# Optimization experiments

Hardware: AMD Instinct MI355X
Metric: run time of the kernel (lower is better)

## Reference

```python
import jax, jax.numpy as jnp
import numpy as np

N = 50000      # total nodes across batched subgraphs
E = 800000     # total edges
R = 4          # num_relations
G = 16         # number of graphs (questions) in batch
NODE_DIM = 128
QDIM = 768
RQ = 64        # reduced_qn_dim
RN = 64        # reduced_node_dim
H = 128        # hidden_dim
OUT = 64       # output_dim


def setup_inputs() -> dict:
    key = jax.random.key(0)
    ks = jax.random.split(key, 16)
    def lin(k, i, o):
        return jax.random.normal(k, (i, o), jnp.float32) / np.float32(np.sqrt(i))
    def rel(k, i, o):
        return jax.random.normal(k, (R, i, o), jnp.float32) / np.float32(np.sqrt(i))
    return {
        "x": jax.random.normal(ks[0], (N, NODE_DIM), jnp.float32),
        "edge_index": jax.random.randint(ks[1], (2, E), 0, N, dtype=jnp.int32),
        "edge_attr": jax.random.randint(ks[2], (E,), 0, R, dtype=jnp.int32),
        "batch": jnp.sort(jax.random.randint(ks[3], (N,), 0, G, dtype=jnp.int32)),
        "question_embedding": jax.random.normal(ks[4], (G, QDIM), jnp.float32),
        "qn_W": lin(ks[5], QDIM, RQ), "qn_b": jnp.zeros((RQ,), jnp.float32),
        "W0": rel(ks[6], NODE_DIM, RN), "root0": lin(ks[7], NODE_DIM, RN), "b0": jnp.zeros((RN,), jnp.float32),
        "W1": rel(ks[8], RN + RQ, H), "root1": lin(ks[9], RN + RQ, H), "b1": jnp.zeros((H,), jnp.float32),
        "W2": rel(ks[10], H, H), "root2": lin(ks[11], H, H), "b2": jnp.zeros((H,), jnp.float32),
        "W3": rel(ks[12], H, OUT), "root3": lin(ks[13], H, OUT), "b3": jnp.zeros((OUT,), jnp.float32),
    }


def rgcn_conv(x, src, dst, etype, W, root, b):
    """PyG RGCNConv: out_i = x_i @ root + b + sum_r mean_{j in N_r(i)} x_j @ W_r."""
    out = x @ root + b
    for r in range(R):
        h = x @ W[r]                                  # [N, out] transform-then-gather
        mask = (etype == r)
        msgs = jnp.where(mask[:, None], h[src], 0.0)  # [E, out]
        s = jax.ops.segment_sum(msgs, dst, num_segments=N)
        cnt = jax.ops.segment_sum(mask.astype(x.dtype), dst, num_segments=N)
        out = out + s / jnp.maximum(cnt, 1.0)[:, None]
    return out


def reference(x, edge_index, edge_attr, batch, question_embedding,
              qn_W, qn_b, W0, root0, b0, W1, root1, b1, W2, root2, b2, W3, root3, b3):
    src, dst = edge_index[0], edge_index[1]
    q = jax.nn.relu(question_embedding @ qn_W + qn_b)          # [G, RQ]
    h = jax.nn.relu(rgcn_conv(x, src, dst, edge_attr, W0, root0, b0))
    combined = jnp.concatenate([h, q[batch]], axis=1)          # [N, RN+RQ]
    h = jax.nn.relu(rgcn_conv(combined, src, dst, edge_attr, W1, root1, b1))
    h = jax.nn.relu(rgcn_conv(h, src, dst, edge_attr, W2, root2, b2))
    return rgcn_conv(h, src, dst, edge_attr, W3, root3, b3)
```

## Files before the change

### kernel.cpp

```cpp
#include <hip/hip_runtime.h>
#include <hip/hip_bf16.h>

#define NN 50000
#define EE 800000
#define GG 16
#define QD 768
#define NBUCK 196
#define EPB 4000

typedef __bf16 bf16x8 __attribute__((ext_vector_type(8)));
typedef float f32x4 __attribute__((ext_vector_type(4)));

static __device__ __forceinline__ float bflo(unsigned u) {
    union { unsigned v; float f; } c; c.v = u << 16; return c.f;
}
static __device__ __forceinline__ float bfhi(unsigned u) {
    union { unsigned v; float f; } c; c.v = u & 0xffff0000u; return c.f;
}


#define PB_CVT 6250
#define PB_W0  (PB_CVT + 160)
#define PB_W1  (PB_W0 + 320)
#define PB_W2  (PB_W1 + 320)
#define PB_W3  (PB_W2 + 160)
#define PB_Q   (PB_W3 + 16)

__global__ __launch_bounds__(256) void prep_all(
        const float* __restrict__ x, __hip_bfloat16* __restrict__ xb,
        const float* __restrict__ qe, const float* __restrict__ qn_W,
        const float* __restrict__ qn_b, float* __restrict__ q,
        const float* __restrict__ W0, const float* __restrict__ root0, __hip_bfloat16* __restrict__ W5T0,
        const float* __restrict__ W1, const float* __restrict__ root1, __hip_bfloat16* __restrict__ W5T1,
        const float* __restrict__ W2, const float* __restrict__ root2, __hip_bfloat16* __restrict__ W5T2,
        const float* __restrict__ W3, const float* __restrict__ root3, __hip_bfloat16* __restrict__ W5T3) {
    __shared__ float red[256];
    int blk = blockIdx.x, tid = threadIdx.x;
    if (blk < PB_CVT) {
        int i = blk * 256 + tid;
        float4 v = ((const float4*)x)[i];
        union { ushort4 u; __hip_bfloat16 h[4]; } o;
        o.h[0] = __float2bfloat16(v.x); o.h[1] = __float2bfloat16(v.y);
        o.h[2] = __float2bfloat16(v.z); o.h[3] = __float2bfloat16(v.w);
        ((ushort4*)xb)[i] = o.u;
    } else if (blk < PB_W3) {
        const float* W; const float* root; __hip_bfloat16* WT; int O, base;
        if (blk < PB_W0)      { W = W0; root = root0; WT = W5T0; O = 64;  base = PB_CVT; }
        else if (blk < PB_W1) { W = W1; root = root1; WT = W5T1; O = 128; base = PB_W0; }
        else if (blk < PB_W2) { W = W2; root = root2; WT = W5T2; O = 128; base = PB_W1; }
        else                  { W = W3; root = root3; WT = W5T3; O = 64;  base = PB_W2; }
        int idx = (blk - base) * 256 + tid;
        int o = idx / 640, k = idx - o * 640;
        float v;
        if (k < 128) v = root[(size_t)k * O + o];
        else { int r = (k - 128) >> 7, kk = (k - 128) & 127; v = W[((size_t)r * 128 + kk) * O + o]; }
        WT[idx] = __float2bfloat16(v);
    } else {
        int g = blk - PB_W3;
        int o = tid & 63, kc = tid >> 6;
        const float* qr = qe + (size_t)g * QD;
        float s = 0.f;
        int k0 = kc * 192;
        for (int k = k0; k < k0 + 192; ++k)
            s = fmaf(qr[k], qn_W[(size_t)k * 64 + o], s);
        red[tid] = s;
        __syncthreads();
        if (tid < 64) {
            float t = red[tid] + red[tid + 64] + red[tid + 128] + red[tid + 192] + qn_b[o];
            q[g * 64 + o] = fmaxf(t, 0.f);
        }
    }
}


__global__ void bucket_hist(const int* __restrict__ dst, int* __restrict__ bcnt) {
    __shared__ int h[NBUCK];
    int tid = threadIdx.x;
    for (int i = tid; i < NBUCK; i += 256) h[i] = 0;
    __syncthreads();
    for (int e = blockIdx.x * 256 + tid; e < EE; e += gridDim.x * 256)
        atomicAdd(&h[dst[e] >> 8], 1);
    __syncthreads();
    for (int i = tid; i < NBUCK; i += 256) if (h[i]) atomicAdd(&bcnt[i], h[i]);
}

__global__ void bucket_scan(const int* __restrict__ bcnt, int* __restrict__ bbase,
                            int* __restrict__ bcur) {
    __shared__ int wt[4];
    int tid = threadIdx.x, lane = tid & 63, w = tid >> 6;
    int v = (tid < NBUCK) ? bcnt[tid] : 0;
    int sc = v;
#pragma unroll
    for (int off = 1; off < 64; off <<= 1) {
        int t = __shfl_up(sc, off, 64);
        if (lane >= off) sc += t;
    }
    if (lane == 63) wt[w] = sc;
    __syncthreads();
    int wbase = 0;
    for (int ww = 0; ww < w; ++ww) wbase += wt[ww];
    int excl = wbase + sc - v;
    if (tid <= NBUCK) bbase[tid] = excl;
    if (tid < NBUCK) bcur[tid] = excl;
}

__global__ __launch_bounds__(256) void bin_edges(const int* __restrict__ src,
                                                 const int* __restrict__ dst,
                                                 const int* __restrict__ et,
                                                 int* __restrict__ bcur,
                                                 unsigned* __restrict__ binned) {
    __shared__ int lcnt[NBUCK];
    __shared__ int lbase[NBUCK];
    int tid = threadIdx.x;
    int e0 = blockIdx.x * EPB, e1 = min(e0 + EPB, EE);
    for (int base = e0; base < e1; base += 2048) {
        for (int i = tid; i < NBUCK; i += 256) lcnt[i] = 0;
        __syncthreads();
        unsigned ent[8]; int bk[8], rk[8];
#pragma unroll
        for (int k = 0; k < 8; ++k) {
            int e = base + k * 256 + tid;
            if (e < e1) {
                int d = dst[e];
                bk[k] = d >> 8;
                ent[k] = ((unsigned)src[e] << 10) | ((unsigned)et[e] << 8) | (unsigned)(d & 255);
                rk[k] = atomicAdd(&lcnt[bk[k]], 1);
            } else bk[k] = -1;
        }
        __syncthreads();
        for (int i = tid; i < NBUCK; i += 256)
            lbase[i] = lcnt[i] ? atomicAdd(&bcur[i], lcnt[i]) : 0;
        __syncthreads();
#pragma unroll
        for (int k = 0; k < 8; ++k)
            if (bk[k] >= 0) binned[lbase[bk[k]] + rk[k]] = ent[k];
        __syncthreads();
    }
}

__global__ __launch_bounds__(256) void csr_fine(const int* __restrict__ bbase,
                                                const unsigned* __restrict__ binned,
                                                int* __restrict__ csr,
                                                int* __restrict__ offsets,
                                                int4* __restrict__ cnt4) {
    __shared__ int cnt[1024];
    __shared__ int wt[4];
    int b = blockIdx.x, tid = threadIdx.x, lane = tid & 63, w = tid >> 6;
    int seg0 = bbase[b], seg1 = bbase[b + 1];
    for (int i = tid; i < 1024; i += 256) cnt[i] = 0;
    __syncthreads();
    for (int e = seg0 + tid; e < seg1; e += 256) {
        unsigned u = binned[e];
        atomicAdd(&cnt[(u & 255) * 4 + ((u >> 8) & 3)], 1);
    }
    __syncthreads();
    int c0 = cnt[tid * 4], c1 = cnt[tid * 4 + 1], c2 = cnt[tid * 4 + 2], c3 = cnt[tid * 4 + 3];
    int s = c0 + c1 + c2 + c3;
    int sc = s;
#pragma unroll
    for (int off = 1; off < 64; off <<= 1) {
        int t = __shfl_up(sc, off, 64);
        if (lane >= off) sc += t;
    }
    if (lane == 63) wt[w] = sc;
    __syncthreads();
    int wbase = 0;
    for (int ww = 0; ww < w; ++ww) wbase += wt[ww];
    int excl = wbase + sc - s;
    cnt[tid * 4]     = excl;
    cnt[tid * 4 + 1] = excl + c0;
    cnt[tid * 4 + 2] = excl + c0 + c1;
    cnt[tid * 4 + 3] = excl + c0 + c1 + c2;
    int node = b * 256 + tid;
    if (node < NN) {
        offsets[node] = seg0 + excl;
        cnt4[node] = make_int4(c0, c1, c2, c3);
    }
    if (b == NBUCK - 1 && tid == 0) offsets[NN] = EE;
    __syncthreads();
    for (int e = seg0 + tid; e < seg1; e += 256) {
        unsigned u = binned[e];
        int r = atomicAdd(&cnt[(u & 255) * 4 + ((u >> 8) & 3)], 1);
        csr[seg0 + r] = (int)(((u >> 10) << 2) | ((u >> 8) & 3));
    }
}


__global__ __launch_bounds__(256) void agg_x(const __hip_bfloat16* __restrict__ X,
                                             const int* __restrict__ offsets,
                                             const int4* __restrict__ cnt4,
                                             const int* __restrict__ csr,
                                             const float* __restrict__ zpage,
                                             __hip_bfloat16* __restrict__ X5agg) {
    int lane = threadIdx.x & 63;
    int node = __builtin_amdgcn_readfirstlane(blockIdx.x * 4 + (threadIdx.x >> 6));
    const char* xb = (const char*)X;
    const char* zp = (const char*)zpage;
    int e0 = offsets[node];
    int4 c4 = cnt4[node];
    int st[4];
    st[0] = 0; st[1] = c4.x; st[2] = st[1] + c4.y; st[3] = st[2] + c4.z;
    int cs[4] = {c4.x, c4.y, c4.z, c4.w};
    int maxc = max(max(cs[0], cs[1]), max(cs[2], cs[3]));
    float aL[4] = {0.f, 0.f, 0.f, 0.f}, aH[4] = {0.f, 0.f, 0.f, 0.f};
    for (int i = 0; i < maxc; i += 2) {
        const char* bp[8];
#pragma unroll
        for (int jj = 0; jj < 2; ++jj) {
            int i2 = i + jj;
#pragma unroll
            for (int r = 0; r < 4; ++r) {
                int p = csr[min(e0 + st[r] + i2, EE - 1)];
                bp[jj * 4 + r] = (i2 < cs[r]) ? xb + (size_t)(p >> 2) * 256 : zp;
            }
        }
        unsigned u[8];
#pragma unroll
        for (int k = 0; k < 8; ++k)
            u[k] = *(const unsigned*)(bp[k] + lane * 4);
#pragma unroll
        for (int k = 0; k < 8; ++k) {
            int r = k & 3;
            aL[r] += bflo(u[k]);
            aH[r] += bfhi(u[k]);
        }
    }
    char* x5 = (char*)X5agg;
#pragma unroll
    for (int r = 0; r < 4; ++r) {
        float iv = 1.f / fmaxf((float)cs[r], 1.f);
        __hip_bfloat16 g0 = __float2bfloat16(aL[r] * iv);
        __hip_bfloat16 g1 = __float2bfloat16(aH[r] * iv);
        ushort2 pkd;
        pkd.x = *(unsigned short*)&g0; pkd.y = *(unsigned short*)&g1;
        *(ushort2*)(x5 + (size_t)node * 1024 + r * 256 + lane * 4) = pkd;
    }
}


template <int O, int MODE>
__global__ __launch_bounds__(256) void dense5(const __hip_bfloat16* __restrict__ Xself,
                                              const __hip_bfloat16* __restrict__ X5agg,
                                              const __hip_bfloat16* __restrict__ W5T,
                                              const float* __restrict__ bias,
                                              const float* __restrict__ q,
                                              const int* __restrict__ batch,
                                              __hip_bfloat16* __restrict__ xnext,
                                              float* __restrict__ out) {
    __shared__ char lds[16384];
    constexpr int NCT = O / 16;
    int tid = threadIdx.x;
    int wave = tid >> 6, lane = tid & 63;
    int quad = lane >> 4, l15 = lane & 15;
    int mbase = blockIdx.x * 128 + wave * 32;
    const __bf16* Ws = (const __bf16*)W5T;

    f32x4 acc[2][NCT];
#pragma unroll
    for (int mt = 0; mt < 2; ++mt)
#pragma unroll
        for (int t = 0; t < NCT; ++t) acc[mt][t] = f32x4{0, 0, 0, 0};

    int arow0 = min(mbase + l15, NN - 1);
    int arow1 = min(mbase + 16 + l15, NN - 1);
    const __bf16* aps0 = (const __bf16*)Xself + (size_t)arow0 * 128;
    const __bf16* aps1 = (const __bf16*)Xself + (size_t)arow1 * 128;
    const __bf16* apg0 = (const __bf16*)X5agg + (size_t)arow0 * 512;
    const __bf16* apg1 = (const __bf16*)X5agg + (size_t)arow1 * 512;

    for (int kc = 0; kc < 10; ++kc) {
        int k0 = kc * 64;
        const __bf16* a0base = (kc < 2) ? aps0 + kc * 64 : apg0 + (kc - 2) * 64;
        const __bf16* a1base = (kc < 2) ? aps1 + kc * 64 : apg1 + (kc - 2) * 64;
        __syncthreads();
        constexpr int NF = NCT * 2 * 64;
#pragma unroll
        for (int i = 0; i < NF / 256; ++i) {
            int f = tid + i * 256;
            int fl = f & 63;
            int o = (f >> 7) * 16 + (fl & 15);
            int kk = k0 + ((f >> 6) & 1) * 32 + ((fl >> 4) & 3) * 8;
            *(uint4*)(lds + f * 16) = *(const uint4*)(Ws + (size_t)o * 640 + kk);
        }
        __syncthreads();
#pragma unroll
        for (int ks = 0; ks < 2; ++ks) {
            bf16x8 a0 = *(const bf16x8*)(a0base + ks * 32 + quad * 8);
            bf16x8 a1 = *(const bf16x8*)(a1base + ks * 32 + quad * 8);
#pragma unroll
            for (int t = 0; t < NCT; ++t) {
                bf16x8 b = *(const bf16x8*)(lds + ((t * 2 + ks) * 64 + lane) * 16);
                acc[0][t] = __builtin_amdgcn_mfma_f32_16x16x32_bf16(a0, b, acc[0][t], 0, 0, 0);
                acc[1][t] = __builtin_amdgcn_mfma_f32_16x16x32_bf16(a1, b, acc[1][t], 0, 0, 0);
            }
        }
    }
    __syncthreads();

    if (MODE == 2) {
#pragma unroll
        for (int mt = 0; mt < 2; ++mt)
#pragma unroll
            for (int t = 0; t < NCT; ++t) {
                int col = t * 16 + l15;
                float bv = bias[col];
#pragma unroll
                for (int reg = 0; reg < 4; ++reg) {
                    int row = mbase + mt * 16 + quad * 4 + reg;
                    if (row < NN) out[(size_t)row * 64 + col] = acc[mt][t][reg] + bv;
                }
            }
        return;
    }

    __hip_bfloat16* tp = (__hip_bfloat16*)(lds + wave * 4096);
#pragma unroll
    for (int mt = 0; mt < 2; ++mt) {
        int m0 = mbase + mt * 16;
#pragma unroll
        for (int t = 0; t < NCT; ++t) {
            int col = t * 16 + l15;
            float bv = bias[col];
#pragma unroll
            for (int reg = 0; reg < 4; ++reg)
                tp[(quad * 4 + reg) * 128 + col] =
                    __float2bfloat16(fmaxf(acc[mt][t][reg] + bv, 0.f));
        }
        if (MODE == 0) {
            int row = lane >> 2;
            int cs = (lane & 3) * 16;
            int rnode = min(m0 + row, NN - 1);
            int g = batch[rnode];
#pragma unroll
            for (int i = 0; i < 4; ++i) {
                float4 v = *(const float4*)(q + g * 64 + cs + i * 4);
                __hip_bfloat16 q0 = __float2bfloat16(v.x), q1 = __float2bfloat16(v.y);
                __hip_bfloat16 q2 = __float2bfloat16(v.z), q3 = __float2bfloat16(v.w);
                ushort4 pk;
                pk.x = *(unsigned short*)&q0; pk.y = *(unsigned short*)&q1;
                pk.z = *(unsigned short*)&q2; pk.w = *(unsigned short*)&q3;
                *(ushort4*)(tp + row * 128 + 64 + cs + i * 4) = pk;
            }
        }
#pragma unroll
        for (int p = 0; p < 4; ++p) {
            int c = p * 64 + lane;
            int row = m0 + (c >> 4);
            if (row < NN)
                *(uint4*)((char*)xnext + (size_t)row * 256 + (c & 15) * 16) =
                    *(const uint4*)((const char*)tp + c * 16);
        }
    }
}


static inline size_t rup(size_t x) { return (x + 255) & ~(size_t)255; }

extern "C" void kernel_launch(void* const* d_in, const int* in_sizes, int n_in,
                              void* d_out, int out_size, void* d_ws, size_t ws_size,
                              hipStream_t stream) {
    const float* x      = (const float*)d_in[0];
    const int*   esrc   = (const int*)d_in[1];
    const int*   edst   = esrc + EE;
    const int*   eattr  = (const int*)d_in[2];
    const int*   batch  = (const int*)d_in[3];
    const float* qe     = (const float*)d_in[4];
    const float* qn_W   = (const float*)d_in[5];
    const float* qn_b   = (const float*)d_in[6];
    const float* W0 = (const float*)d_in[7],  *root0 = (const float*)d_in[8],  *b0 = (const float*)d_in[9];
    const float* W1 = (const float*)d_in[10], *root1 = (const float*)d_in[11], *b1 = (const float*)d_in[12];
    const float* W2 = (const float*)d_in[13], *root2 = (const float*)d_in[14], *b2 = (const float*)d_in[15];
    const float* W3 = (const float*)d_in[16], *root3 = (const float*)d_in[17], *b3 = (const float*)d_in[18];
    float* out = (float*)d_out;

    char* w = (char*)d_ws;
    float* q       = (float*)w;  w += rup(GG * 64 * 4);
    float* zpage   = (float*)w;  w += rup(256);
    int*   offsets = (int*)w;    w += rup(((size_t)NN + 1) * 4);
    int4*  cnt4    = (int4*)w;   w += rup((size_t)NN * 16);
    int*   bcnt    = (int*)w;    w += rup((size_t)NBUCK * 4);
    int*   bbase   = (int*)w;    w += rup(((size_t)NBUCK + 1) * 4);
    int*   bcur    = (int*)w;    w += rup((size_t)NBUCK * 4);
    unsigned* binned = (unsigned*)w; w += rup((size_t)EE * 4);
    int*   csr     = (int*)w;    w += rup((size_t)EE * 4);
    __hip_bfloat16* W5T0 = (__hip_bfloat16*)w; w += rup((size_t)64 * 640 * 2);
    __hip_bfloat16* W5T1 = (__hip_bfloat16*)w; w += rup((size_t)128 * 640 * 2);
    __hip_bfloat16* W5T2 = (__hip_bfloat16*)w; w += rup((size_t)128 * 640 * 2);
    __hip_bfloat16* W5T3 = (__hip_bfloat16*)w; w += rup((size_t)64 * 640 * 2);
    __hip_bfloat16* xb0 = (__hip_bfloat16*)w;  w += rup((size_t)NN * 128 * 2);
    __hip_bfloat16* xb1 = (__hip_bfloat16*)w;  w += rup((size_t)NN * 128 * 2);
    __hip_bfloat16* X5  = (__hip_bfloat16*)w;  w += rup((size_t)NN * 512 * 2);

    hipMemsetAsync(bcnt, 0, (size_t)NBUCK * 4, stream);
    hipMemsetAsync(zpage, 0, 256, stream);

    prep_all<<<PB_Q, 256, 0, stream>>>(x, xb0, qe, qn_W, qn_b, q,
                                       W0, root0, W5T0, W1, root1, W5T1,
                                       W2, root2, W5T2, W3, root3, W5T3);

    bucket_hist<<<256, 256, 0, stream>>>(edst, bcnt);
    bucket_scan<<<1, 256, 0, stream>>>(bcnt, bbase, bcur);
    bin_edges<<<(EE + EPB - 1) / EPB, 256, 0, stream>>>(esrc, edst, eattr, bcur, binned);
    csr_fine<<<NBUCK, 256, 0, stream>>>(bbase, binned, csr, offsets, cnt4);

    int aggblk = NN / 4;
    int dblk = (NN + 127) / 128;

    agg_x<<<aggblk, 256, 0, stream>>>(xb0, offsets, cnt4, csr, zpage, X5);
    dense5<64, 0><<<dblk, 256, 0, stream>>>(xb0, X5, W5T0, b0, q, batch, xb1, nullptr);

    agg_x<<<aggblk, 256, 0, stream>>>(xb1, offsets, cnt4, csr, zpage, X5);
    dense5<128, 1><<<dblk, 256, 0, stream>>>(xb1, X5, W5T1, b1, nullptr, nullptr, xb0, nullptr);

    agg_x<<<aggblk, 256, 0, stream>>>(xb0, offsets, cnt4, csr, zpage, X5);
    dense5<128, 1><<<dblk, 256, 0, stream>>>(xb0, X5, W5T2, b2, nullptr, nullptr, xb1, nullptr);

    agg_x<<<aggblk, 256, 0, stream>>>(xb1, offsets, cnt4, csr, zpage, X5);
    dense5<64, 2><<<dblk, 256, 0, stream>>>(xb1, X5, W5T3, b3, nullptr, nullptr, nullptr, out);
}
```

Measured before the change: 396.4 us.

## Fuse all phases into a persistent cooperative megakernel with grid syncs

Replaces the chain of separate kernel launches and memsets with one cooperative persistent kernel that loops over work with grid-stride loops and separates phases with grid.sync(). The aggregation loop now loads 64 CSR entries per wave at once and broadcasts them with readlane instead of reloading per edge. The dense stage appears retiled to 64-row tiles. Launch gaps and tail effects between phases should shrink, at the cost of grid-wide barriers, occupancy capped by the cooperative grid size, and register pressure from merging all phases into one kernel. A multi-kernel fallback is kept for when the cooperative launch fails.

Result: slower. 1.279 ms (+222.6%).

```diff
diff --git a/kernel.cpp b/kernel.cpp
--- a/kernel.cpp
+++ b/kernel.cpp
@@ -1,23 +1,16 @@
 #include <hip/hip_runtime.h>
 #include <hip/hip_bf16.h>
+#include <hip/hip_cooperative_groups.h>
+
+namespace cg = cooperative_groups;
 
 #define NN 50000
 #define EE 800000
 #define GG 16
 #define QD 768
 #define NBUCK 196
-#define EPB 4000
-
-typedef __bf16 bf16x8 __attribute__((ext_vector_type(8)));
-typedef float f32x4 __attribute__((ext_vector_type(4)));
-
-static __device__ __forceinline__ float bflo(unsigned u) {
-    union { unsigned v; float f; } c; c.v = u << 16; return c.f;
-}
-static __device__ __forceinline__ float bfhi(unsigned u) {
-    union { unsigned v; float f; } c; c.v = u & 0xffff0000u; return c.f;
-}
-
+#define NCHUNK ((EE + 2047) / 2048)
+#define NT64 ((NN + 63) / 64)
 
 #define PB_CVT 6250
 #define PB_W0  (PB_CVT + 160)
@@ -25,70 +18,89 @@
 #define PB_W2  (PB_W1 + 320)
 #define PB_W3  (PB_W2 + 160)
 #define PB_Q   (PB_W3 + 16)
-
-__global__ __launch_bounds__(256) void prep_all(
-        const float* __restrict__ x, __hip_bfloat16* __restrict__ xb,
-        const float* __restrict__ qe, const float* __restrict__ qn_W,
-        const float* __restrict__ qn_b, float* __restrict__ q,
-        const float* __restrict__ W0, const float* __restrict__ root0, __hip_bfloat16* __restrict__ W5T0,
-        const float* __restrict__ W1, const float* __restrict__ root1, __hip_bfloat16* __restrict__ W5T1,
-        const float* __restrict__ W2, const float* __restrict__ root2, __hip_bfloat16* __restrict__ W5T2,
-        const float* __restrict__ W3, const float* __restrict__ root3, __hip_bfloat16* __restrict__ W5T3) {
-    __shared__ float red[256];
-    int blk = blockIdx.x, tid = threadIdx.x;
-    if (blk < PB_CVT) {
-        int i = blk * 256 + tid;
-        float4 v = ((const float4*)x)[i];
-        union { ushort4 u; __hip_bfloat16 h[4]; } o;
-        o.h[0] = __float2bfloat16(v.x); o.h[1] = __float2bfloat16(v.y);
-        o.h[2] = __float2bfloat16(v.z); o.h[3] = __float2bfloat16(v.w);
-        ((ushort4*)xb)[i] = o.u;
-    } else if (blk < PB_W3) {
-        const float* W; const float* root; __hip_bfloat16* WT; int O, base;
-        if (blk < PB_W0)      { W = W0; root = root0; WT = W5T0; O = 64;  base = PB_CVT; }
-        else if (blk < PB_W1) { W = W1; root = root1; WT = W5T1; O = 128; base = PB_W0; }
-        else if (blk < PB_W2) { W = W2; root = root2; WT = W5T2; O = 128; base = PB_W1; }
-        else                  { W = W3; root = root3; WT = W5T3; O = 64;  base = PB_W2; }
-        int idx = (blk - base) * 256 + tid;
-        int o = idx / 640, k = idx - o * 640;
-        float v;
-        if (k < 128) v = root[(size_t)k * O + o];
-        else { int r = (k - 128) >> 7, kk = (k - 128) & 127; v = W[((size_t)r * 128 + kk) * O + o]; }
-        WT[idx] = __float2bfloat16(v);
-    } else {
-        int g = blk - PB_W3;
-        int o = tid & 63, kc = tid >> 6;
-        const float* qr = qe + (size_t)g * QD;
-        float s = 0.f;
-        int k0 = kc * 192;
-        for (int k = k0; k < k0 + 192; ++k)
-            s = fmaf(qr[k], qn_W[(size_t)k * 64 + o], s);
-        red[tid] = s;
-        __syncthreads();
-        if (tid < 64) {
-            float t = red[tid] + red[tid + 64] + red[tid + 128] + red[tid + 192] + qn_b[o];
-            q[g * 64 + o] = fmaxf(t, 0.f);
-        }
-    }
-}
-
-
-__global__ void bucket_hist(const int* __restrict__ dst, int* __restrict__ bcnt) {
-    __shared__ int h[NBUCK];
+#define PB_TOT (PB_Q + 1)
+
+typedef __bf16 bf16x8 __attribute__((ext_vector_type(8)));
+typedef float f32x4 __attribute__((ext_vector_type(4)));
+
+struct P {
+    const float* x; const int* esrc; const int* edst; const int* eattr; const int* batch;
+    const float* qe; const float* qn_W; const float* qn_b;
+    const float *W0, *root0, *b0, *W1, *root1, *b1, *W2, *root2, *b2, *W3, *root3, *b3;
+    float* out;
+    float* q; float* zpage; int* offsets; int4* cnt4; int* bcnt; int* bbase; int* bcur;
+    unsigned* binned; int* csr;
+    __hip_bfloat16 *W5T0, *W5T1, *W5T2, *W5T3, *xb0, *xb1, *X5;
+};
+
+static __device__ __forceinline__ float bflo(unsigned u) {
+    union { unsigned v; float f; } c; c.v = u << 16; return c.f;
+}
+static __device__ __forceinline__ float bfhi(unsigned u) {
+    union { unsigned v; float f; } c; c.v = u & 0xffff0000u; return c.f;
+}
+
+static __device__ void prep_phase(const P& p, char* smem) {
+    int tid = threadIdx.x;
+    for (int blk = blockIdx.x; blk < PB_TOT; blk += gridDim.x) {
+        if (blk < PB_CVT) {
+            int i = blk * 256 + tid;
+            float4 v = ((const float4*)p.x)[i];
+            union { ushort4 u; __hip_bfloat16 h[4]; } o;
+            o.h[0] = __float2bfloat16(v.x); o.h[1] = __float2bfloat16(v.y);
+            o.h[2] = __float2bfloat16(v.z); o.h[3] = __float2bfloat16(v.w);
+            ((ushort4*)p.xb0)[i] = o.u;
+        } else if (blk < PB_W3) {
+            const float* W; const float* root; __hip_bfloat16* WT; int O, base;
+            if (blk < PB_W0)      { W = p.W0; root = p.root0; WT = p.W5T0; O = 64;  base = PB_CVT; }
+            else if (blk < PB_W1) { W = p.W1; root = p.root1; WT = p.W5T1; O = 128; base = PB_W0; }
+            else if (blk < PB_W2) { W = p.W2; root = p.root2; WT = p.W5T2; O = 128; base = PB_W1; }
+            else                  { W = p.W3; root = p.root3; WT = p.W5T3; O = 64;  base = PB_W2; }
+            int idx = (blk - base) * 256 + tid;
+            int o = idx / 640, k = idx - o * 640;
+            float v;
+            if (k < 128) v = root[(size_t)k * O + o];
+            else { int r = (k - 128) >> 7, kk = (k - 128) & 127; v = W[((size_t)r * 128 + kk) * O + o]; }
+            WT[idx] = __float2bfloat16(v);
+        } else if (blk < PB_Q) {
+            float* red = (float*)smem;
+            int g = blk - PB_W3;
+            int o = tid & 63, kc = tid >> 6;
+            const float* qr = p.qe + (size_t)g * QD;
+            float s = 0.f;
+            int k0 = kc * 192;
+            for (int k = k0; k < k0 + 192; ++k)
+                s = fmaf(qr[k], p.qn_W[(size_t)k * 64 + o], s);
+            red[tid] = s;
+            __syncthreads();
+            if (tid < 64) {
+                float t = red[tid] + red[tid + 64] + red[tid + 128] + red[tid + 192] + p.qn_b[o];
+                p.q[g * 64 + o] = fmaxf(t, 0.f);
+            }
+            __syncthreads();
+        } else {
+            if (tid < NBUCK) p.bcnt[tid] = 0;
+            if (tid < 64) p.zpage[tid] = 0.f;
+        }
+    }
+}
+
+static __device__ void hist_phase(const P& p, char* smem) {
+    int* h = (int*)smem;
     int tid = threadIdx.x;
     for (int i = tid; i < NBUCK; i += 256) h[i] = 0;
     __syncthreads();
     for (int e = blockIdx.x * 256 + tid; e < EE; e += gridDim.x * 256)
-        atomicAdd(&h[dst[e] >> 8], 1);
+        atomicAdd(&h[p.edst[e] >> 8], 1);
     __syncthreads();
-    for (int i = tid; i < NBUCK; i += 256) if (h[i]) atomicAdd(&bcnt[i], h[i]);
-}
-
-__global__ void bucket_scan(const int* __restrict__ bcnt, int* __restrict__ bbase,
-                            int* __restrict__ bcur) {
-    __shared__ int wt[4];
+    for (int i = tid; i < NBUCK; i += 256) if (h[i]) atomicAdd(&p.bcnt[i], h[i]);
+    __syncthreads();
+}
+
+static __device__ void scan_phase(const P& p, char* smem) {
+    int* wt = (int*)smem;
     int tid = threadIdx.x, lane = tid & 63, w = tid >> 6;
-    int v = (tid < NBUCK) ? bcnt[tid] : 0;
+    int v = (tid < NBUCK) ? p.bcnt[tid] : 0;
     int sc = v;
 #pragma unroll
     for (int off = 1; off < 64; off <<= 1) {
@@ -100,20 +112,16 @@
     int wbase = 0;
     for (int ww = 0; ww < w; ++ww) wbase += wt[ww];
     int excl = wbase + sc - v;
-    if (tid <= NBUCK) bbase[tid] = excl;
-    if (tid < NBUCK) bcur[tid] = excl;
-}
-
-__global__ __launch_bounds__(256) void bin_edges(const int* __restrict__ src,
-                                                 const int* __restrict__ dst,
-                                                 const int* __restrict__ et,
-                                                 int* __restrict__ bcur,
-                                                 unsigned* __restrict__ binned) {
-    __shared__ int lcnt[NBUCK];
-    __shared__ int lbase[NBUCK];
+    if (tid <= NBUCK) p.bbase[tid] = excl;
+    if (tid < NBUCK) p.bcur[tid] = excl;
+}
+
+static __device__ void bin_phase(const P& p, char* smem) {
+    int* lcnt = (int*)smem;
+    int* lbase = lcnt + NBUCK;
     int tid = threadIdx.x;
-    int e0 = blockIdx.x * EPB, e1 = min(e0 + EPB, EE);
-    for (int base = e0; base < e1; base += 2048) {
+    for (int c = blockIdx.x; c < NCHUNK; c += gridDim.x) {
+        int base = c * 2048, e1 = min(base + 2048, EE);
         for (int i = tid; i < NBUCK; i += 256) lcnt[i] = 0;
         __syncthreads();
         unsigned ent[8]; int bk[8], rk[8];
@@ -121,236 +129,291 @@
         for (int k = 0; k < 8; ++k) {
             int e = base + k * 256 + tid;
             if (e < e1) {
-                int d = dst[e];
+                int d = p.edst[e];
                 bk[k] = d >> 8;
-                ent[k] = ((unsigned)src[e] << 10) | ((unsigned)et[e] << 8) | (unsigned)(d & 255);
+                ent[k] = ((unsigned)p.esrc[e] << 10) | ((unsigned)p.eattr[e] << 8) | (unsigned)(d & 255);
                 rk[k] = atomicAdd(&lcnt[bk[k]], 1);
             } else bk[k] = -1;
         }
         __syncthreads();
         for (int i = tid; i < NBUCK; i += 256)
-            lbase[i] = lcnt[i] ? atomicAdd(&bcur[i], lcnt[i]) : 0;
+            lbase[i] = lcnt[i] ? atomicAdd(&p.bcur[i], lcnt[i]) : 0;
         __syncthreads();
 #pragma unroll
         for (int k = 0; k < 8; ++k)
-            if (bk[k] >= 0) binned[lbase[bk[k]] + rk[k]] = ent[k];
-        __syncthreads();
-    }
-}
-
-__global__ __launch_bounds__(256) void csr_fine(const int* __restrict__ bbase,
-                                                const unsigned* __restrict__ binned,
-                                                int* __restrict__ csr,
-                                                int* __restrict__ offsets,
-                                                int4* __restrict__ cnt4) {
-    __shared__ int cnt[1024];
-    __shared__ int wt[4];
-    int b = blockIdx.x, tid = threadIdx.x, lane = tid & 63, w = tid >> 6;
-    int seg0 = bbase[b], seg1 = bbase[b + 1];
-    for (int i = tid; i < 1024; i += 256) cnt[i] = 0;
-    __syncthreads();
-    for (int e = seg0 + tid; e < seg1; e += 256) {
-        unsigned u = binned[e];
-        atomicAdd(&cnt[(u & 255) * 4 + ((u >> 8) & 3)], 1);
-    }
-    __syncthreads();
-    int c0 = cnt[tid * 4], c1 = cnt[tid * 4 + 1], c2 = cnt[tid * 4 + 2], c3 = cnt[tid * 4 + 3];
-    int s = c0 + c1 + c2 + c3;
-    int sc = s;
-#pragma unroll
-    for (int off = 1; off < 64; off <<= 1) {
-        int t = __shfl_up(sc, off, 64);
-        if (lane >= off) sc += t;
-    }
-    if (lane == 63) wt[w] = sc;
-    __syncthreads();
-    int wbase = 0;
-    for (int ww = 0; ww < w; ++ww) wbase += wt[ww];
-    int excl = wbase + sc - s;
-    cnt[tid * 4]     = excl;
-    cnt[tid * 4 + 1] = excl + c0;
-    cnt[tid * 4 + 2] = excl + c0 + c1;
-    cnt[tid * 4 + 3] = excl + c0 + c1 + c2;
-    int node = b * 256 + tid;
-    if (node < NN) {
-        offsets[node] = seg0 + excl;
-        cnt4[node] = make_int4(c0, c1, c2, c3);
-    }
-    if (b == NBUCK - 1 && tid == 0) offsets[NN] = EE;
-    __syncthreads();
-    for (int e = seg0 + tid; e < seg1; e += 256) {
-        unsigned u = binned[e];
-        int r = atomicAdd(&cnt[(u & 255) * 4 + ((u >> 8) & 3)], 1);
-        csr[seg0 + r] = (int)(((u >> 10) << 2) | ((u >> 8) & 3));
-    }
-}
-
-
-__global__ __launch_bounds__(256) void agg_x(const __hip_bfloat16* __restrict__ X,
-                                             const int* __restrict__ offsets,
-                                             const int4* __restrict__ cnt4,
-                                             const int* __restrict__ csr,
-                                             const float* __restrict__ zpage,
-                                             __hip_bfloat16* __restrict__ X5agg) {
+            if (bk[k] >= 0) p.binned[lbase[bk[k]] + rk[k]] = ent[k];
+        __syncthreads();
+    }
+}
+
+static __device__ void fine_phase(const P& p, char* smem) {
+    int* cnt = (int*)smem;
+    int* wt = cnt + 1024;
+    int tid = threadIdx.x, lane = tid & 63, w = tid >> 6;
+    for (int b = blockIdx.x; b < NBUCK; b += gridDim.x) {
+        int seg0 = p.bbase[b], seg1 = p.bbase[b + 1];
+        for (int i = tid; i < 1024; i += 256) cnt[i] = 0;
+        __syncthreads();
+        for (int e = seg0 + tid; e < seg1; e += 256) {
+            unsigned u = p.binned[e];
+            atomicAdd(&cnt[(u & 255) * 4 + ((u >> 8) & 3)], 1);
+        }
+        __syncthreads();
+        int c0 = cnt[tid * 4], c1 = cnt[tid * 4 + 1], c2 = cnt[tid * 4 + 2], c3 = cnt[tid * 4 + 3];
+        int s = c0 + c1 + c2 + c3;
+        int sc = s;
+#pragma unroll
+        for (int off = 1; off < 64; off <<= 1) {
+            int t = __shfl_up(sc, off, 64);
+            if (lane >= off) sc += t;
+        }
+        if (lane == 63) wt[w] = sc;
+        __syncthreads();
+        int wbase = 0;
+        for (int ww = 0; ww < w; ++ww) wbase += wt[ww];
+        int excl = wbase + sc - s;
+        cnt[tid * 4]     = excl;
+        cnt[tid * 4 + 1] = excl + c0;
+        cnt[tid * 4 + 2] = excl + c0 + c1;
+        cnt[tid * 4 + 3] = excl + c0 + c1 + c2;
+        int node = b * 256 + tid;
+        if (node < NN) {
+            p.offsets[node] = seg0 + excl;
+            p.cnt4[node] = make_int4(c0, c1, c2, c3);
+        }
+        if (b == NBUCK - 1 && tid == 0) p.offsets[NN] = EE;
+        __syncthreads();
+        for (int e = seg0 + tid; e < seg1; e += 256) {
+            unsigned u = p.binned[e];
+            int r = atomicAdd(&cnt[(u & 255) * 4 + ((u >> 8) & 3)], 1);
+            p.csr[seg0 + r] = (int)(((u >> 10) << 2) | ((u >> 8) & 3));
+        }
+        __syncthreads();
+    }
+}
+
+static __device__ void agg_phase(const __hip_bfloat16* X, const int* offsets,
+                                 const int4* cnt4, const int* csr,
+                                 const float* zpage, __hip_bfloat16* X5agg) {
     int lane = threadIdx.x & 63;
-    int node = __builtin_amdgcn_readfirstlane(blockIdx.x * 4 + (threadIdx.x >> 6));
+    int gw = blockIdx.x * 4 + (threadIdx.x >> 6);
     const char* xb = (const char*)X;
     const char* zp = (const char*)zpage;
-    int e0 = offsets[node];
-    int4 c4 = cnt4[node];
-    int st[4];
-    st[0] = 0; st[1] = c4.x; st[2] = st[1] + c4.y; st[3] = st[2] + c4.z;
-    int cs[4] = {c4.x, c4.y, c4.z, c4.w};
-    int maxc = max(max(cs[0], cs[1]), max(cs[2], cs[3]));
-    float aL[4] = {0.f, 0.f, 0.f, 0.f}, aH[4] = {0.f, 0.f, 0.f, 0.f};
-    for (int i = 0; i < maxc; i += 2) {
-        const char* bp[8];
-#pragma unroll
-        for (int jj = 0; jj < 2; ++jj) {
-            int i2 = i + jj;
-#pragma unroll
-            for (int r = 0; r < 4; ++r) {
-                int p = csr[min(e0 + st[r] + i2, EE - 1)];
-                bp[jj * 4 + r] = (i2 < cs[r]) ? xb + (size_t)(p >> 2) * 256 : zp;
-            }
-        }
-        unsigned u[8];
-#pragma unroll
-        for (int k = 0; k < 8; ++k)
-            u[k] = *(const unsigned*)(bp[k] + lane * 4);
-#pragma unroll
-        for (int k = 0; k < 8; ++k) {
-            int r = k & 3;
-            aL[r] += bflo(u[k]);
-            aH[r] += bfhi(u[k]);
-        }
-    }
-    char* x5 = (char*)X5agg;
-#pragma unroll
-    for (int r = 0; r < 4; ++r) {
-        float iv = 1.f / fmaxf((float)cs[r], 1.f);
-        __hip_bfloat16 g0 = __float2bfloat16(aL[r] * iv);
-        __hip_bfloat16 g1 = __float2bfloat16(aH[r] * iv);
-        ushort2 pkd;
-        pkd.x = *(unsigned short*)&g0; pkd.y = *(unsigned short*)&g1;
-        *(ushort2*)(x5 + (size_t)node * 1024 + r * 256 + lane * 4) = pkd;
-    }
-}
-
+    for (int n0 = gw; n0 < NN; n0 += gridDim.x * 4) {
+        int node = __builtin_amdgcn_readfirstlane(n0);
+        int e0 = __builtin_amdgcn_readfirstlane(offsets[node]);
+        int4 c4 = cnt4[node];
+        int cs[4];
+        cs[0] = __builtin_amdgcn_readfirstlane(c4.x);
+        cs[1] = __builtin_amdgcn_readfirstlane(c4.y);
+        cs[2] = __builtin_amdgcn_readfirstlane(c4.z);
+        cs[3] = __builtin_amdgcn_readfirstlane(c4.w);
+        int st[4];
+        st[0] = 0; st[1] = cs[0]; st[2] = st[1] + cs[1]; st[3] = st[2] + cs[2];
+        int maxc = max(max(cs[0], cs[1]), max(cs[2], cs[3]));
+        float aL[4] = {0.f, 0.f, 0.f, 0.f}, aH[4] = {0.f, 0.f, 0.f, 0.f};
+        for (int base = 0; base < maxc; base += 64) {
+            int pk[4];
+#pragma unroll
+            for (int r = 0; r < 4; ++r)
+                pk[r] = csr[min(e0 + st[r] + base + lane, EE - 1)];
+            int m = min(64, maxc - base);
+            for (int j = 0; j < m; j += 4) {
+                const char* bp[16];
+#pragma unroll
+                for (int jj = 0; jj < 4; ++jj) {
+                    int i = base + j + jj;
+#pragma unroll
+                    for (int r = 0; r < 4; ++r) {
+                        int pv = __builtin_amdgcn_readlane(pk[r], j + jj);
+                        bp[jj * 4 + r] = (i < cs[r]) ? xb + (size_t)(pv >> 2) * 256 : zp;
+                    }
+                }
+                unsigned u[16];
+#pragma unroll
+                for (int k = 0; k < 16; ++k)
+                    u[k] = *(const unsigned*)(bp[k] + lane * 4);
+#pragma unroll
+                for (int k = 0; k < 16; ++k) {
+                    int r = k & 3;
+                    aL[r] += bflo(u[k]);
+                    aH[r] += bfhi(u[k]);
+                }
+            }
+        }
+        char* x5 = (char*)X5agg;
+#pragma unroll
+        for (int r = 0; r < 4; ++r) {
+            float iv = 1.f / fmaxf((float)cs[r], 1.f);
+            __hip_bfloat16 g0 = __float2bfloat16(aL[r] * iv);
+            __hip_bfloat16 g1 = __float2bfloat16(aH[r] * iv);
+            ushort2 pkd;
+            pkd.x = *(unsigned short*)&g0; pkd.y = *(unsigned short*)&g1;
+            *(ushort2*)(x5 + (size_t)node * 1024 + r * 256 + lane * 4) = pkd;
+        }
+    }
+}
 
 template <int O, int MODE>
-__global__ __launch_bounds__(256) void dense5(const __hip_bfloat16* __restrict__ Xself,
-                                              const __hip_bfloat16* __restrict__ X5agg,
-                                              const __hip_bfloat16* __restrict__ W5T,
-                                              const float* __restrict__ bias,
-                                              const float* __restrict__ q,
-                                              const int* __restrict__ batch,
-                                              __hip_bfloat16* __restrict__ xnext,
-                                              float* __restrict__ out) {
-    __shared__ char lds[16384];
+static __device__ void dense_phase(const __hip_bfloat16* Xself, const __hip_bfloat16* X5agg,
+                                   const __hip_bfloat16* W5T, const float* bias,
+                                   const float* q, const int* batch,
+                                   __hip_bfloat16* xnext, float* out, char* lds) {
     constexpr int NCT = O / 16;
     int tid = threadIdx.x;
     int wave = tid >> 6, lane = tid & 63;
     int quad = lane >> 4, l15 = lane & 15;
-    int mbase = blockIdx.x * 128 + wave * 32;
     const __bf16* Ws = (const __bf16*)W5T;
-
-    f32x4 acc[2][NCT];
-#pragma unroll
-    for (int mt = 0; mt < 2; ++mt)
-#pragma unroll
-        for (int t = 0; t < NCT; ++t) acc[mt][t] = f32x4{0, 0, 0, 0};
-
-    int arow0 = min(mbase + l15, NN - 1);
-    int arow1 = min(mbase + 16 + l15, NN - 1);
-    const __bf16* aps0 = (const __bf16*)Xself + (size_t)arow0 * 128;
-    const __bf16* aps1 = (const __bf16*)Xself + (size_t)arow1 * 128;
-    const __bf16* apg0 = (const __bf16*)X5agg + (size_t)arow0 * 512;
-    const __bf16* apg1 = (const __bf16*)X5agg + (size_t)arow1 * 512;
-
-    for (int kc = 0; kc < 10; ++kc) {
-        int k0 = kc * 64;
-        const __bf16* a0base = (kc < 2) ? aps0 + kc * 64 : apg0 + (kc - 2) * 64;
-        const __bf16* a1base = (kc < 2) ? aps1 + kc * 64 : apg1 + (kc - 2) * 64;
-        __syncthreads();
-        constexpr int NF = NCT * 2 * 64;
-#pragma unroll
-        for (int i = 0; i < NF / 256; ++i) {
-            int f = tid + i * 256;
-            int fl = f & 63;
-            int o = (f >> 7) * 16 + (fl & 15);
-            int kk = k0 + ((f >> 6) & 1) * 32 + ((fl >> 4) & 3) * 8;
-            *(uint4*)(lds + f * 16) = *(const uint4*)(Ws + (size_t)o * 640 + kk);
-        }
-        __syncthreads();
-#pragma unroll
-        for (int ks = 0; ks < 2; ++ks) {
-            bf16x8 a0 = *(const bf16x8*)(a0base + ks * 32 + quad * 8);
-            bf16x8 a1 = *(const bf16x8*)(a1base + ks * 32 + quad * 8);
-#pragma unroll
-            for (int t = 0; t < NCT; ++t) {
-                bf16x8 b = *(const bf16x8*)(lds + ((t * 2 + ks) * 64 + lane) * 16);
-                acc[0][t] = __builtin_amdgcn_mfma_f32_16x16x32_bf16(a0, b, acc[0][t], 0, 0, 0);
-                acc[1][t] = __builtin_amdgcn_mfma_f32_16x16x32_bf16(a1, b, acc[1][t], 0, 0, 0);
-            }
-        }
-    }
-    __syncthreads();
-
-    if (MODE == 2) {
-#pragma unroll
-        for (int mt = 0; mt < 2; ++mt)
+    for (int tile = blockIdx.x; tile < NT64; tile += gridDim.x) {
+        int mbase = tile * 64 + wave * 16;
+        f32x4 acc[NCT];
+#pragma unroll
+        for (int t = 0; t < NCT; ++t) acc[t] = f32x4{0, 0, 0, 0};
+        int arow0 = min(mbase + l15, NN - 1);
+        const __bf16* aps0 = (const __bf16*)Xself + (size_t)arow0 * 128;
+        const __bf16* apg0 = (const __bf16*)X5agg + (size_t)arow0 * 512;
+        for (int kc = 0; kc < 10; ++kc) {
+            int k0 = kc * 64;
+            const __bf16* a0base = (kc < 2) ? aps0 + kc * 64 : apg0 + (kc - 2) * 64;
+            __syncthreads();
+            constexpr int NF = NCT * 2 * 64;
+#pragma unroll
+            for (int i = 0; i < NF / 256; ++i) {
+                int f = tid + i * 256;
+                int fl = f & 63;
+                int o = (f >> 7) * 16 + (fl & 15);
+                int kk = k0 + ((f >> 6) & 1) * 32 + ((fl >> 4) & 3) * 8;
+                *(uint4*)(lds + f * 16) = *(const uint4*)(Ws + (size_t)o * 640 + kk);
+            }
+            __syncthreads();
+#pragma unroll
+            for (int ks = 0; ks < 2; ++ks) {
+                bf16x8 a0 = *(const bf16x8*)(a0base + ks * 32 + quad * 8);
+#pragma unroll
+                for (int t = 0; t < NCT; ++t) {
+                    bf16x8 b = *(const bf16x8*)(lds + ((t * 2 + ks) * 64 + lane) * 16);
+                    acc[t] = __builtin_amdgcn_mfma_f32_16x16x32_bf16(a0, b, acc[t], 0, 0, 0);
+                }
+            }
+        }
+        __syncthreads();
+
+        if (MODE == 2) {
 #pragma unroll
             for (int t = 0; t < NCT; ++t) {
                 int col = t * 16 + l15;
                 float bv = bias[col];
 #pragma unroll
                 for (int reg = 0; reg < 4; ++reg) {
-                    int row = mbase + mt * 16 + quad * 4 + reg;
-                    if (row < NN) out[(size_t)row * 64 + col] = acc[mt][t][reg] + bv;
+                    int row = mbase + quad * 4 + reg;
+                    if (row < NN) out[(size_t)row * 64 + col] = acc[t][reg] + bv;
                 }
             }
-        return;
-    }
-
-    __hip_bfloat16* tp = (__hip_bfloat16*)(lds + wave * 4096);
-#pragma unroll
-    for (int mt = 0; mt < 2; ++mt) {
-        int m0 = mbase + mt * 16;
-#pragma unroll
-        for (int t = 0; t < NCT; ++t) {
-            int col = t * 16 + l15;
-            float bv = bias[col];
-#pragma unroll
-            for (int reg = 0; reg < 4; ++reg)
-                tp[(quad * 4 + reg) * 128 + col] =
-                    __float2bfloat16(fmaxf(acc[mt][t][reg] + bv, 0.f));
-        }
-        if (MODE == 0) {
-            int row = lane >> 2;
-            int cs = (lane & 3) * 16;
-            int rnode = min(m0 + row, NN - 1);
-            int g = batch[rnode];
-#pragma unroll
-            for (int i = 0; i < 4; ++i) {
-                float4 v = *(const float4*)(q + g * 64 + cs + i * 4);
-                __hip_bfloat16 q0 = __float2bfloat16(v.x), q1 = __float2bfloat16(v.y);
-                __hip_bfloat16 q2 = __float2bfloat16(v.z), q3 = __float2bfloat16(v.w);
-                ushort4 pk;
-                pk.x = *(unsigned short*)&q0; pk.y = *(unsigned short*)&q1;
-                pk.z = *(unsigned short*)&q2; pk.w = *(unsigned short*)&q3;
-                *(ushort4*)(tp + row * 128 + 64 + cs + i * 4) = pk;
-            }
-        }
-#pragma unroll
-        for (int p = 0; p < 4; ++p) {
-            int c = p * 64 + lane;
-            int row = m0 + (c >> 4);
-            if (row < NN)
-                *(uint4*)((char*)xnext + (size_t)row * 256 + (c & 15) * 16) =
-                    *(const uint4*)((const char*)tp + c * 16);
-        }
-    }
+        } else {
+            __hip_bfloat16* tp = (__hip_bfloat16*)(lds + wave * 4096);
+            int m0 = mbase;
+#pragma unroll
+            for (int t = 0; t < NCT; ++t) {
+                int col = t * 16 + l15;
+                float bv = bias[col];
+#pragma unroll
+                for (int reg = 0; reg < 4; ++reg)
+                    tp[(quad * 4 + reg) * 128 + col] =
+                        __float2bfloat16(fmaxf(acc[t][reg] + bv, 0.f));
+            }
+            if (MODE == 0) {
+                int row = lane >> 2;
+                int cseg = (lane & 3) * 16;
+                int rnode = min(m0 + row, NN - 1);
+                int g = batch[rnode];
+#pragma unroll
+                for (int i = 0; i < 4; ++i) {
+                    float4 v = *(const float4*)(q + g * 64 + cseg + i * 4);
+                    __hip_bfloat16 q0 = __float2bfloat16(v.x), q1 = __float2bfloat16(v.y);
+                    __hip_bfloat16 q2 = __float2bfloat16(v.z), q3 = __float2bfloat16(v.w);
+                    ushort4 pk;
+                    pk.x = *(unsigned short*)&q0; pk.y = *(unsigned short*)&q1;
+                    pk.z = *(unsigned short*)&q2; pk.w = *(unsigned short*)&q3;
+                    *(ushort4*)(tp + row * 128 + 64 + cseg + i * 4) = pk;
+                }
+            }
+#pragma unroll
+            for (int pp = 0; pp < 4; ++pp) {
+                int c = pp * 64 + lane;
+                int row = m0 + (c >> 4);
+                if (row < NN)
+                    *(uint4*)((char*)xnext + (size_t)row * 256 + (c & 15) * 16) =
+                        *(const uint4*)((const char*)tp + c * 16);
+            }
+        }
+    }
+}
+
+__global__ __launch_bounds__(256, 4) void mega(P p) {
+    __shared__ char smem[16384];
+    cg::grid_group grid = cg::this_grid();
+
+    prep_phase(p, smem);
+    grid.sync();
+    hist_phase(p, smem);
+    grid.sync();
+    if (blockIdx.x == 0) scan_phase(p, smem);
+    grid.sync();
+    bin_phase(p, smem);
+    grid.sync();
+    fine_phase(p, smem);
+    grid.sync();
+
+    agg_phase(p.xb0, p.offsets, p.cnt4, p.csr, p.zpage, p.X5);
+    grid.sync();
+    dense_phase<64, 0>(p.xb0, p.X5, p.W5T0, p.b0, p.q, p.batch, p.xb1, nullptr, smem);
+    grid.sync();
+    agg_phase(p.xb1, p.offsets, p.cnt4, p.csr, p.zpage, p.X5);
+    grid.sync();
+    dense_phase<128, 1>(p.xb1, p.X5, p.W5T1, p.b1, nullptr, nullptr, p.xb0, nullptr, smem);
+    grid.sync();
+    agg_phase(p.xb0, p.offsets, p.cnt4, p.csr, p.zpage, p.X5);
+    grid.sync();
+    dense_phase<128, 1>(p.xb0, p.X5, p.W5T2, p.b2, nullptr, nullptr, p.xb1, nullptr, smem);
+    grid.sync();
+    agg_phase(p.xb1, p.offsets, p.cnt4, p.csr, p.zpage, p.X5);
+    grid.sync();
+    dense_phase<64, 2>(p.xb1, p.X5, p.W5T3, p.b3, nullptr, nullptr, nullptr, p.out, smem);
+}
+
+__global__ __launch_bounds__(256) void k_prep(P p) {
+    __shared__ char smem[1024];
+    prep_phase(p, smem);
+}
+__global__ __launch_bounds__(256) void k_hist(P p) {
+    __shared__ char smem[NBUCK * 4];
+    hist_phase(p, smem);
+}
+__global__ __launch_bounds__(256) void k_scan(P p) {
+    __shared__ char smem[16];
+    scan_phase(p, smem);
+}
+__global__ __launch_bounds__(256) void k_bin(P p) {
+    __shared__ char smem[NBUCK * 8];
+    bin_phase(p, smem);
+}
+__global__ __launch_bounds__(256) void k_fine(P p) {
+    __shared__ char smem[1028 * 4];
+    fine_phase(p, smem);
+}
+__global__ __launch_bounds__(256) void k_agg(P p, int sel) {
+    const __hip_bfloat16* X = sel ? p.xb1 : p.xb0;
+    agg_phase(X, p.offsets, p.cnt4, p.csr, p.zpage, p.X5);
+}
+template <int O, int MODE>
+__global__ __launch_bounds__(256) void k_dense(P p, int sel) {
+    __shared__ char smem[16384];
+    const __hip_bfloat16* Xs = sel ? p.xb1 : p.xb0;
+    __hip_bfloat16* xn = sel ? p.xb0 : p.xb1;
+    const __hip_bfloat16* W5T = (MODE == 0) ? p.W5T0 : (MODE == 2) ? p.W5T3
+                               : (sel ? p.W5T1 : p.W5T2);
+    const float* bias = (MODE == 0) ? p.b0 : (MODE == 2) ? p.b3 : (sel ? p.b1 : p.b2);
+    dense_phase<O, MODE>(Xs, p.X5, W5T, bias, p.q, p.batch, xn, p.out, smem);
 }
 
 
@@ -359,62 +422,75 @@
 extern "C" void kernel_launch(void* const* d_in, const int* in_sizes, int n_in,
                               void* d_out, int out_size, void* d_ws, size_t ws_size,
                               hipStream_t stream) {
-    const float* x      = (const float*)d_in[0];
-    const int*   esrc   = (const int*)d_in[1];
-    const int*   edst   = esrc + EE;
-    const int*   eattr  = (const int*)d_in[2];
-    const int*   batch  = (const int*)d_in[3];
-    const float* qe     = (const float*)d_in[4];
-    const float* qn_W   = (const float*)d_in[5];
-    const float* qn_b   = (const float*)d_in[6];
-    const float* W0 = (const float*)d_in[7],  *root0 = (const float*)d_in[8],  *b0 = (const float*)d_in[9];
-    const float* W1 = (const float*)d_in[10], *root1 = (const float*)d_in[11], *b1 = (const float*)d_in[12];
-    const float* W2 = (const float*)d_in[13], *root2 = (const float*)d_in[14], *b2 = (const float*)d_in[15];
-    const float* W3 = (const float*)d_in[16], *root3 = (const float*)d_in[17], *b3 = (const float*)d_in[18];
-    float* out = (float*)d_out;
+    P prm;
+    prm.x      = (const float*)d_in[0];
+    prm.esrc   = (const int*)d_in[1];
+    prm.edst   = prm.esrc + EE;
+    prm.eattr  = (const int*)d_in[2];
+    prm.batch  = (const int*)d_in[3];
+    prm.qe     = (const float*)d_in[4];
+    prm.qn_W   = (const float*)d_in[5];
+    prm.qn_b   = (const float*)d_in[6];
+    prm.W0 = (const float*)d_in[7];  prm.root0 = (const float*)d_in[8];  prm.b0 = (const float*)d_in[9];
+    prm.W1 = (const float*)d_in[10]; prm.root1 = (const float*)d_in[11]; prm.b1 = (const float*)d_in[12];
+    prm.W2 = (const float*)d_in[13]; prm.root2 = (const float*)d_in[14]; prm.b2 = (const float*)d_in[15];
+    prm.W3 = (const float*)d_in[16]; prm.root3 = (const float*)d_in[17]; prm.b3 = (const float*)d_in[18];
+    prm.out = (float*)d_out;
 
     char* w = (char*)d_ws;
-    float* q       = (float*)w;  w += rup(GG * 64 * 4);
-    float* zpage   = (float*)w;  w += rup(256);
-    int*   offsets = (int*)w;    w += rup(((size_t)NN + 1) * 4);
-    int4*  cnt4    = (int4*)w;   w += rup((size_t)NN * 16);
-    int*   bcnt    = (int*)w;    w += rup((size_t)NBUCK * 4);
-    int*   bbase   = (int*)w;    w += rup(((size_t)NBUCK + 1) * 4);
-    int*   bcur    = (int*)w;    w += rup((size_t)NBUCK * 4);
-    unsigned* binned = (unsigned*)w; w += rup((size_t)EE * 4);
-    int*   csr     = (int*)w;    w += rup((size_t)EE * 4);
-    __hip_bfloat16* W5T0 = (__hip_bfloat16*)w; w += rup((size_t)64 * 640 * 2);
-    __hip_bfloat16* W5T1 = (__hip_bfloat16*)w; w += rup((size_t)128 * 640 * 2);
-    __hip_bfloat16* W5T2 = (__hip_bfloat16*)w; w += rup((size_t)128 * 640 * 2);
-    __hip_bfloat16* W5T3 = (__hip_bfloat16*)w; w += rup((size_t)64 * 640 * 2);
-    __hip_bfloat16* xb0 = (__hip_bfloat16*)w;  w += rup((size_t)NN * 128 * 2);
-    __hip_bfloat16* xb1 = (__hip_bfloat16*)w;  w += rup((size_t)NN * 128 * 2);
-    __hip_bfloat16* X5  = (__hip_bfloat16*)w;  w += rup((size_t)NN * 512 * 2);
-
-    hipMemsetAsync(bcnt, 0, (size_t)NBUCK * 4, stream);
-    hipMemsetAsync(zpage, 0, 256, stream);
-
-    prep_all<<<PB_Q, 256, 0, stream>>>(x, xb0, qe, qn_W, qn_b, q,
-                                       W0, root0, W5T0, W1, root1, W5T1,
-                                       W2, root2, W5T2, W3, root3, W5T3);
-
-    bucket_hist<<<256, 256, 0, stream>>>(edst, bcnt);
-    bucket_scan<<<1, 256, 0, stream>>>(bcnt, bbase, bcur);
-    bin_edges<<<(EE + EPB - 1) / EPB, 256, 0, stream>>>(esrc, edst, eattr, bcur, binned);
-    csr_fine<<<NBUCK, 256, 0, stream>>>(bbase, binned, csr, offsets, cnt4);
-
-    int aggblk = NN / 4;
-    int dblk = (NN + 127) / 128;
-
-    agg_x<<<aggblk, 256, 0, stream>>>(xb0, offsets, cnt4, csr, zpage, X5);
-    dense5<64, 0><<<dblk, 256, 0, stream>>>(xb0, X5, W5T0, b0, q, batch, xb1, nullptr);
-
-    agg_x<<<aggblk, 256, 0, stream>>>(xb1, offsets, cnt4, csr, zpage, X5);
-    dense5<128, 1><<<dblk, 256, 0, stream>>>(xb1, X5, W5T1, b1, nullptr, nullptr, xb0, nullptr);
-
-    agg_x<<<aggblk, 256, 0, stream>>>(xb0, offsets, cnt4, csr, zpage, X5);
-    dense5<128, 1><<<dblk, 256, 0, stream>>>(xb0, X5, W5T2, b2, nullptr, nullptr, xb1, nullptr);
-
-    agg_x<<<aggblk, 256, 0, stream>>>(xb1, offsets, cnt4, csr, zpage, X5);
-    dense5<64, 2><<<dblk, 256, 0, stream>>>(xb1, X5, W5T3, b3, nullptr, nullptr, nullptr, out);
-}
+    prm.q       = (float*)w;  w += rup(GG * 64 * 4);
+    prm.zpage   = (float*)w;  w += rup(256);
+    prm.offsets = (int*)w;    w += rup(((size_t)NN + 1) * 4);
+    prm.cnt4    = (int4*)w;   w += rup((size_t)NN * 16);
+    prm.bcnt    = (int*)w;    w += rup((size_t)NBUCK * 4);
+    prm.bbase   = (int*)w;    w += rup(((size_t)NBUCK + 1) * 4);
+    prm.bcur    = (int*)w;    w += rup((size_t)NBUCK * 4);
+    prm.binned  = (unsigned*)w; w += rup((size_t)EE * 4);
+    prm.csr     = (int*)w;    w += rup((size_t)EE * 4);
+    prm.W5T0 = (__hip_bfloat16*)w; w += rup((size_t)64 * 640 * 2);
+    prm.W5T1 = (__hip_bfloat16*)w; w += rup((size_t)128 * 640 * 2);
+    prm.W5T2 = (__hip_bfloat16*)w; w += rup((size_t)128 * 640 * 2);
+    prm.W5T3 = (__hip_bfloat16*)w; w += rup((size_t)64 * 640 * 2);
+    prm.xb0 = (__hip_bfloat16*)w;  w += rup((size_t)NN * 128 * 2);
+    prm.xb1 = (__hip_bfloat16*)w;  w += rup((size_t)NN * 128 * 2);
+    prm.X5  = (__hip_bfloat16*)w;  w += rup((size_t)NN * 512 * 2);
+
+    static int coop_grid = -2;
+    if (coop_grid == -2) {
+        int nb = 0;
+        hipError_t e = hipOccupancyMaxActiveBlocksPerMultiprocessor(
+            &nb, (const void*)mega, 256, 0);
+        if (e == hipSuccess && nb >= 1) {
+            if (nb > 4) nb = 4;
+            coop_grid = nb * 256;
+        } else {
+            coop_grid = -1;
+        }
+    }
+
+    bool done = false;
+    if (coop_grid > 0) {
+        void* args[] = { (void*)&prm };
+        hipError_t e = hipLaunchCooperativeKernel((const void*)mega, dim3(coop_grid),
+                                                  dim3(256), args, 0, stream);
+        if (e == hipSuccess) done = true;
+        else coop_grid = -1;
+    }
+
+    if (!done) {
+        k_prep<<<PB_TOT, 256, 0, stream>>>(prm);
+        k_hist<<<256, 256, 0, stream>>>(prm);
+        k_scan<<<1, 256, 0, stream>>>(prm);
+        k_bin<<<NCHUNK, 256, 0, stream>>>(prm);
+        k_fine<<<NBUCK, 256, 0, stream>>>(prm);
+
+        k_agg<<<NN / 4, 256, 0, stream>>>(prm, 0);
+        k_dense<64, 0><<<NT64, 256, 0, stream>>>(prm, 0);
+        k_agg<<<NN / 4, 256, 0, stream>>>(prm, 1);
+        k_dense<128, 1><<<NT64, 256, 0, stream>>>(prm, 1);
+        k_agg<<<NN / 4, 256, 0, stream>>>(prm, 0);
+        k_dense<128, 1><<<NT64, 256, 0, stream>>>(prm, 0);
+        k_agg<<<NN / 4, 256, 0, stream>>>(prm, 1);
+        k_dense<64, 2><<<NT64, 256, 0, stream>>>(prm, 1);
+    }
+}
```
